# Kernel tuning notes

Hardware: AMD Instinct MI355X
Metric: run time of the kernel (lower is better)

## Reference

```python
import jax, jax.numpy as jnp
import numpy as np

B = 16384       # batch size
P = 2           # fixed pooling factor per bag (offsets are arange * P)
NTAB = 26       # number of sparse feature tables
NROWS = 100000  # rows per embedding table
D = 128         # embedding dim == ln_bot[-1]
LN_BOT = [13, 512, 256, 128]
LN_TOP = [479, 1024, 512, 256, 1]


def setup_inputs() -> dict:
    key = jax.random.key(0)
    ks = jax.random.split(key, 32)
    inp = {}
    inp['dense_x'] = jax.random.normal(ks[0], (B, LN_BOT[0]), dtype=jnp.float32)
    # offsets: uniform stride-P bags (EmbeddingBag offsets)
    inp['lS_o'] = jnp.broadcast_to(jnp.arange(B, dtype=jnp.int64) * P, (NTAB, B))
    inp['lS_i'] = jax.random.randint(ks[1], (NTAB, B * P), 0, NROWS, dtype=jnp.int64)
    # embedding tables, uniform(-sqrt(1/n), sqrt(1/n))
    bound = float(np.sqrt(1.0 / NROWS))
    inp['emb_tables'] = jax.random.uniform(ks[2], (NTAB, NROWS, D), dtype=jnp.float32,
                                           minval=-bound, maxval=bound)
    # bot MLP params (He-style scaled normal)
    ki = 3
    for i in range(len(LN_BOT) - 1):
        n, m = LN_BOT[i], LN_BOT[i + 1]
        inp[f'bw{i}'] = jax.random.normal(ks[ki], (m, n), dtype=jnp.float32) * np.sqrt(2.0 / (m + n)); ki += 1
        inp[f'bb{i}'] = jax.random.normal(ks[ki], (m,), dtype=jnp.float32) * np.sqrt(1.0 / m); ki += 1
    for i in range(len(LN_TOP) - 1):
        n, m = LN_TOP[i], LN_TOP[i + 1]
        inp[f'tw{i}'] = jax.random.normal(ks[ki], (m, n), dtype=jnp.float32) * np.sqrt(2.0 / (m + n)); ki += 1
        inp[f'tb{i}'] = jax.random.normal(ks[ki], (m,), dtype=jnp.float32) * np.sqrt(1.0 / m); ki += 1
    return inp


def _mlp(x, Ws, bs, sigmoid_layer):
    for i, (W, b) in enumerate(zip(Ws, bs)):
        x = x @ W.T + b
        x = jax.nn.sigmoid(x) if i == sigmoid_layer else jax.nn.relu(x)
    return x


def reference(dense_x, lS_o, lS_i, emb_tables,
              bw0, bb0, bw1, bb1, bw2, bb2,
              tw0, tb0, tw1, tb1, tw2, tb2, tw3, tb3):
    # bot MLP (sigmoid_bot = -1 -> all ReLU)
    x = _mlp(dense_x, [bw0, bw1, bw2], [bb0, bb1, bb2], sigmoid_layer=-1)  # [B, D]

    # multi-table EmbeddingBag sum pooling. Offsets (lS_o) are uniform stride-P
    # arange bags, so sum pooling is a gather + reshape + sum over P.
    def pool_one(table, idx):
        return table[idx].reshape(B, P, D).sum(axis=1)  # [B, D]
    ly = jax.vmap(pool_one)(emb_tables, lS_i)  # [NTAB, B, D]

    # dot interaction (arch_interaction_itself=False -> strict lower triangle)
    T = jnp.concatenate([x[:, None, :], jnp.transpose(ly, (1, 0, 2))], axis=1)  # [B, 27, D]
    Z = jnp.einsum('bid,bjd->bij', T, T)  # [B, 27, 27]
    ni = NTAB + 1
    li, lj = jnp.tril_indices(ni, k=-1)
    Zflat = Z[:, li, lj]  # [B, 351]
    R = jnp.concatenate([x, Zflat], axis=1)  # [B, 479]

    # top MLP (sigmoid at last layer, sigmoid_top = 3)
    p = _mlp(R, [tw0, tw1, tw2, tw3], [tb0, tb1, tb2, tb3], sigmoid_layer=3)
    return p  # [B, 1]
```

## Files before the change

### kernel.cpp

```cpp
#include <hip/hip_runtime.h>
#include <hip/hip_bf16.h>
#include <math.h>

#define BATCH 16384
#define NTAB 26
#define DIM 128
#define NROWS 100000

typedef short bf16x8 __attribute__((ext_vector_type(8)));
typedef float f32x4 __attribute__((ext_vector_type(4)));
typedef float f32x16 __attribute__((ext_vector_type(16)));

__device__ __forceinline__ ushort f2b(float f) {
  union { float f; unsigned u; } c; c.f = f;
  unsigned r = (c.u + 0x7fffu + ((c.u >> 16) & 1u)) >> 16;
  return (ushort)r;
}
__device__ __forceinline__ float b2f(ushort u) {
  union { unsigned u; float f; } c; c.u = (unsigned)u << 16;
  return c.f;
}

__device__ __forceinline__ void gload_lds16(const void* g, void* l) {
  __builtin_amdgcn_global_load_lds(
      (const __attribute__((address_space(1))) void*)g,
      (__attribute__((address_space(3))) void*)l, 16, 0, 0);
}

__global__ __launch_bounds__(256) void prep_kernel(
    const float* __restrict__ x, const float* __restrict__ W0,
    const float* __restrict__ b0, ushort* __restrict__ y,
    const float* __restrict__ bw1, const float* __restrict__ bw2,
    const float* __restrict__ tw0, const float* __restrict__ tw1,
    const float* __restrict__ tw2,
    ushort* __restrict__ o1, ushort* __restrict__ o2, ushort* __restrict__ o3,
    ushort* __restrict__ o4, ushort* __restrict__ o5) {
  int blk = blockIdx.x;
  if (blk < 2 * BATCH) {
    int b = blk >> 1;
    int m = ((blk & 1) << 8) | threadIdx.x;
    const float* xr = x + (size_t)b * 13;
    const float* wr = W0 + (size_t)m * 13;
    float acc = b0[m];
#pragma unroll
    for (int k = 0; k < 13; k++) acc = fmaf(xr[k], wr[k], acc);
    y[(size_t)b * 512 + m] = f2b(fmaxf(acc, 0.f));
    return;
  }
  int cb = blk - 2 * BATCH;
  int c = cb >> 11;
  int i = (cb & 2047) * 256 + threadIdx.x;
  switch (c) {
    case 0: if (i < 256 * 512) o1[i] = f2b(bw1[i]); break;
    case 1: if (i < 128 * 256) {
      int r = i >> 8, cc = i & 255;
      int db = (((cc << 1) ^ ((r & 7) << 4)) >> 1);
      o2[r * 256 + db] = f2b(bw2[i]);
    } break;
    case 2: if (i < 1024 * 512) {
      int r = i >> 9, cc = i & 511;
      o3[i] = (cc < 479) ? f2b(tw0[(size_t)r * 479 + cc]) : (ushort)0;
    } break;
    case 3: if (i < 512 * 1024) o4[i] = f2b(tw1[i]); break;
    case 4: if (i < 256 * 512) o5[i] = f2b(tw2[i]); break;
  }
}

__global__ __launch_bounds__(256) void embint_kernel(
    const float* __restrict__ tables, const int* __restrict__ lS_i,
    const ushort* __restrict__ xb, ushort* __restrict__ R) {
  __shared__ ushort Tls[4][32 * 128];
  const int wave = threadIdx.x >> 6, lane = threadIdx.x & 63;
  const int b = blockIdx.x * 4 + wave;
  char* tl = (char*)Tls[wave];

  *(uint*)(tl + lane * 4) = *(const uint*)(xb + (size_t)b * 128 + lane * 2);
#pragma unroll
  for (int r = 27; r < 32; r++)
    *(uint*)(tl + r * 256 + ((lane * 4) ^ ((r & 7) << 4))) = 0;
#pragma unroll 8
  for (int t = 0; t < NTAB; t++) {
    const int* idx = lS_i + ((size_t)t << 15) + (b << 1);
    int i0 = idx[0], i1 = idx[1];
    float2 v0 = ((const float2*)(tables + ((size_t)t * NROWS + i0) * DIM))[lane];
    float2 v1 = ((const float2*)(tables + ((size_t)t * NROWS + i1) * DIM))[lane];
    ushort2 s; s.x = f2b(v0.x + v1.x); s.y = f2b(v0.y + v1.y);
    int row = t + 1;
    *(uint*)(tl + row * 256 + ((lane * 4) ^ ((row & 7) << 4))) = *(uint*)&s;
  }
  __syncthreads();

  const int row = lane & 31;
  const int khb = (lane >> 5) * 16;
  const int swz = (row & 7) << 4;
  f32x16 z = {};
#pragma unroll
  for (int ks = 0; ks < 8; ks++) {
    bf16x8 a = *(const bf16x8*)(tl + row * 256 + ((ks * 32 + khb) ^ swz));
    z = __builtin_amdgcn_mfma_f32_32x32x16_bf16(a, a, z, 0, 0, 0);
  }

  ushort* Rb = R + (size_t)b * 512;
  *(uint*)(Rb + lane * 2) = *(const uint*)(tl + lane * 4);
  if (lane < 33) Rb[479 + lane] = 0;
  const int j = lane & 31;
  const int rb4 = (lane >> 5) * 4;
#pragma unroll
  for (int r = 0; r < 16; r++) {
    int i = (r & 3) + 8 * (r >> 2) + rb4;
    if (i <= 26 && j < i) Rb[DIM + (i * (i - 1)) / 2 + j] = f2b(z[r]);
  }
}

#define BMLP_SLOT 20480
__global__ __launch_bounds__(256) void bmlp_kernel(
    const ushort* __restrict__ A, const ushort* __restrict__ W1,
    const float* __restrict__ b1, const ushort* __restrict__ W2g,
    const float* __restrict__ b2, ushort* __restrict__ Y) {
  __shared__ char lds[3 * BMLP_SLOT + 64 * 260 * 2 + 65536];
  char* C1 = lds + 3 * BMLP_SLOT;
  char* W2s = C1 + 64 * 260 * 2;
  const int tid = threadIdx.x;
  const int lane = tid & 63, wave = tid >> 6;
  const int m0 = blockIdx.x * 64;

  const int srow = lane >> 2;
  const int scolb = ((lane & 3) << 4) ^ ((srow & 3) << 4);

#pragma unroll
  for (int i = 0; i < 16; i++)
    gload_lds16(W2g + i * 2048 + wave * 512 + lane * 8, W2s + i * 4096 + wave * 1024);

#pragma unroll
  for (int kt = 0; kt < 2; kt++) {
    char* As = lds + kt * BMLP_SLOT;
    char* W1s = As + 4096;
    const int k0 = kt * 32;
    gload_lds16(A + (size_t)(m0 + wave * 16 + srow) * 512 + k0 + (scolb >> 1),
                As + wave * 1024);
#pragma unroll
    for (int i = 0; i < 4; i++)
      gload_lds16(W1 + (size_t)(wave * 64 + i * 16 + srow) * 512 + k0 + (scolb >> 1),
                  W1s + wave * 4096 + i * 1024);
  }

  f32x4 acc1[4][4] = {};
  const int fr = lane & 15;
  const int fkb = (lane >> 4) * 16;
  const int fswz = (fr & 3) << 4;

  for (int kt = 0; kt < 16; kt++) {
    if (kt < 15) { asm volatile("s_waitcnt vmcnt(5)" ::: "memory"); }
    else         { asm volatile("s_waitcnt vmcnt(0)" ::: "memory"); }
    __builtin_amdgcn_sched_barrier(0);
    __builtin_amdgcn_s_barrier();
    __builtin_amdgcn_sched_barrier(0);

    const char* As = lds + (kt % 3) * BMLP_SLOT;
    const char* W1s = As + 4096;
    bf16x8 a[4], w[4];
#pragma unroll
    for (int i = 0; i < 4; i++)
      a[i] = *(const bf16x8*)(As + (i * 16 + fr) * 64 + (fkb ^ fswz));
#pragma unroll
    for (int j = 0; j < 4; j++)
      w[j] = *(const bf16x8*)(W1s + (wave * 64 + j * 16 + fr) * 64 + (fkb ^ fswz));

    if (kt + 2 < 16) {
      char* Ad = lds + ((kt + 2) % 3) * BMLP_SLOT;
      char* W1d = Ad + 4096;
      const int k2 = (kt + 2) * 32;
      gload_lds16(A + (size_t)(m0 + wave * 16 + srow) * 512 + k2 + (scolb >> 1),
                  Ad + wave * 1024);
#pragma unroll
      for (int i = 0; i < 4; i++)
        gload_lds16(W1 + (size_t)(wave * 64 + i * 16 + srow) * 512 + k2 + (scolb >> 1),
                    W1d + wave * 4096 + i * 1024);
    }

    asm volatile("s_waitcnt lgkmcnt(0)" ::: "memory");
    __builtin_amdgcn_sched_barrier(0);
    __builtin_amdgcn_s_setprio(1);
#pragma unroll
    for (int i = 0; i < 4; i++)
#pragma unroll
      for (int j = 0; j < 4; j++)
        acc1[i][j] = __builtin_amdgcn_mfma_f32_16x16x32_bf16(a[i], w[j], acc1[i][j], 0, 0, 0);
    __builtin_amdgcn_s_setprio(0);
  }

  const int col_l = lane & 15, row_h = (lane >> 4) * 4;
#pragma unroll
  for (int j = 0; j < 4; j++) {
    int n = wave * 64 + j * 16 + col_l;
    float bs = b1[n];
#pragma unroll
    for (int i = 0; i < 4; i++) {
      int rw = i * 16 + row_h;
#pragma unroll
      for (int r = 0; r < 4; r++)
        *(ushort*)(C1 + (size_t)(rw + r) * 520 + n * 2) = f2b(fmaxf(acc1[i][j][r] + bs, 0.f));
    }
  }
  __syncthreads();

  f32x4 acc2[4][2] = {};
#pragma unroll
  for (int ks = 0; ks < 8; ks++) {
    const int kb = ks * 64 + fkb;
    bf16x8 a2[4], w2[2];
#pragma unroll
    for (int i = 0; i < 4; i++)
      a2[i] = *(const bf16x8*)(C1 + (i * 16 + fr) * 520 + kb);
#pragma unroll
    for (int j = 0; j < 2; j++)
      w2[j] = *(const bf16x8*)(W2s + (wave * 32 + j * 16 + fr) * 512 + (kb ^ ((fr & 7) << 4)));
#pragma unroll
    for (int i = 0; i < 4; i++)
#pragma unroll
      for (int j = 0; j < 2; j++)
        acc2[i][j] = __builtin_amdgcn_mfma_f32_16x16x32_bf16(a2[i], w2[j], acc2[i][j], 0, 0, 0);
  }

#pragma unroll
  for (int j = 0; j < 2; j++) {
    int n = wave * 32 + j * 16 + col_l;
    float bs = b2[n];
#pragma unroll
    for (int i = 0; i < 4; i++) {
      int mb = m0 + i * 16 + row_h;
#pragma unroll
      for (int r = 0; r < 4; r++)
        Y[(size_t)(mb + r) * 128 + n] = f2b(fmaxf(acc2[i][j][r] + bs, 0.f));
    }
  }
}

#define SLOT_BYTES 49152
template <int ACT>
__global__ __launch_bounds__(512, 2) void gemm256_kernel(
    const ushort* __restrict__ A, const ushort* __restrict__ W,
    const float* __restrict__ bias, ushort* __restrict__ C, int K, int ldc) {
  __shared__ char lds[3 * SLOT_BYTES];
  const int tid = threadIdx.x;
  const int lane = tid & 63, wid = tid >> 6;
  const int wm = wid >> 2, wn = wid & 3;

  const int nwg = gridDim.x * gridDim.y;
  const int orig = blockIdx.y * gridDim.x + blockIdx.x;
  const int q = nwg >> 3, r8 = nwg & 7;
  const int xcd = orig & 7, pos = orig >> 3;
  const int swzid = (xcd < r8 ? xcd * (q + 1) : r8 * (q + 1) + (xcd - r8) * q) + pos;
  const int m0 = (swzid / gridDim.x) * 256, n0 = (swzid % gridDim.x) * 128;
  const int NK = K >> 6;

  const int srow = tid >> 3;
  const int scolb = (tid & 7) << 4;

#pragma unroll
  for (int kt = 0; kt < 2; kt++) {
    char* As = lds + kt * SLOT_BYTES;
    char* Bs = As + 32768;
    const int k0 = kt * 64;
#pragma unroll
    for (int i = 0; i < 4; i++) {
      int row = i * 64 + srow;
      int colb = scolb ^ ((row & 7) << 4);
      gload_lds16(A + (size_t)(m0 + row) * K + k0 + (colb >> 1), As + i * 8192 + wid * 1024);
    }
#pragma unroll
    for (int i = 0; i < 2; i++) {
      int row = i * 64 + srow;
      int colb = scolb ^ ((row & 7) << 4);
      gload_lds16(W + (size_t)(n0 + row) * K + k0 + (colb >> 1), Bs + i * 8192 + wid * 1024);
    }
  }

  f32x4 acc[8][2] = {};
  const int fr = lane & 15;
  const int fkb = (lane >> 4) * 16;

  for (int kt = 0; kt < NK; kt++) {
    if (kt + 1 < NK) { asm volatile("s_waitcnt vmcnt(6)" ::: "memory"); }
    else             { asm volatile("s_waitcnt vmcnt(0)" ::: "memory"); }
    __builtin_amdgcn_sched_barrier(0);
    __builtin_amdgcn_s_barrier();
    __builtin_amdgcn_sched_barrier(0);

    const char* As = lds + (kt % 3) * SLOT_BYTES;
    const char* Bs = As + 32768;
    char* Ad = lds + ((kt + 2) % 3) * SLOT_BYTES;
    char* Bd = Ad + 32768;
    const int k2 = (kt + 2) * 64;
    const bool do_stage = (kt + 2 < NK);

#pragma unroll
    for (int kh = 0; kh < 2; kh++) {
      bf16x8 a[8], b[2];
#pragma unroll
      for (int mf = 0; mf < 8; mf++) {
        int row = wm * 128 + mf * 16 + fr;
        int colb = (kh * 64 + fkb) ^ ((row & 7) << 4);
        a[mf] = *(const bf16x8*)(As + row * 128 + colb);
      }
#pragma unroll
      for (int nf = 0; nf < 2; nf++) {
        int row = wn * 32 + nf * 16 + fr;
        int colb = (kh * 64 + fkb) ^ ((row & 7) << 4);
        b[nf] = *(const bf16x8*)(Bs + row * 128 + colb);
      }
      if (do_stage) {
#pragma unroll
        for (int i = kh * 2; i < kh * 2 + 2; i++) {
          int row = i * 64 + srow;
          int colb = scolb ^ ((row & 7) << 4);
          gload_lds16(A + (size_t)(m0 + row) * K + k2 + (colb >> 1), Ad + i * 8192 + wid * 1024);
        }
        {
          int row = kh * 64 + srow;
          int colb = scolb ^ ((row & 7) << 4);
          gload_lds16(W + (size_t)(n0 + row) * K + k2 + (colb >> 1), Bd + kh * 8192 + wid * 1024);
        }
      }
      __builtin_amdgcn_sched_barrier(0);
      __builtin_amdgcn_s_barrier();
      asm volatile("s_waitcnt lgkmcnt(0)" ::: "memory");
      __builtin_amdgcn_sched_barrier(0);
      __builtin_amdgcn_s_setprio(1);
#pragma unroll
      for (int mf = 0; mf < 8; mf++)
#pragma unroll
        for (int nf = 0; nf < 2; nf++)
          acc[mf][nf] = __builtin_amdgcn_mfma_f32_16x16x32_bf16(a[mf], b[nf], acc[mf][nf], 0, 0, 0);
      __builtin_amdgcn_s_setprio(0);
      if (kh == 0) {
        __builtin_amdgcn_sched_barrier(0);
        __builtin_amdgcn_s_barrier();
        __builtin_amdgcn_sched_barrier(0);
      }
    }
  }

  const int cr = lane & 15, rh = (lane >> 4) * 4;
#pragma unroll
  for (int nf = 0; nf < 2; nf++) {
    int n = n0 + wn * 32 + nf * 16 + cr;
    float bs = bias[n];
#pragma unroll
    for (int mf = 0; mf < 8; mf++) {
      int mb = m0 + wm * 128 + mf * 16 + rh;
#pragma unroll
      for (int r = 0; r < 4; r++) {
        float v = acc[mf][nf][r] + bs;
        if (ACT) v = fmaxf(v, 0.f);
        C[(size_t)(mb + r) * ldc + n] = f2b(v);
      }
    }
  }
}

__global__ __launch_bounds__(256) void t2final_kernel(
    const ushort* __restrict__ A, const ushort* __restrict__ W,
    const float* __restrict__ bias, const float* __restrict__ w3,
    const float* __restrict__ b3, float* __restrict__ out) {
  __shared__ char smem[64 * 264 * 2];
  ushort* As = (ushort*)smem;
  ushort* Bs = (ushort*)(smem + 4096);
  ushort* Ct = (ushort*)smem;
  const int tid = threadIdx.x;
  const int lane = tid & 63, wave = tid >> 6;
  const int m0 = blockIdx.x * 64;

  const int srow = lane >> 2;
  const int scolb = ((lane & 3) << 4) ^ ((srow & 3) << 4);
  const ushort* Ag = A + (size_t)(m0 + wave * 16 + srow) * 512 + (scolb >> 1);
  const ushort* Wg = W + (size_t)(wave * 16 + srow) * 512 + (scolb >> 1);

  f32x4 acc[4][4] = {};
  const int fr = lane & 15;
  const int fkb = (lane >> 4) * 16;
  const int fswz = (fr & 3) << 4;

  for (int k0 = 0; k0 < 512; k0 += 32) {
    gload_lds16(Ag + k0, (char*)As + wave * 1024);
#pragma unroll
    for (int i = 0; i < 4; i++)
      gload_lds16(Wg + (size_t)(i * 64) * 512 + k0, (char*)Bs + i * 4096 + wave * 1024);
    __syncthreads();
    bf16x8 a[4], b[4];
#pragma unroll
    for (int i = 0; i < 4; i++) {
      a[i] = *(const bf16x8*)((const char*)As + (i * 16 + fr) * 64 + (fkb ^ fswz));
      b[i] = *(const bf16x8*)((const char*)Bs + (wave * 64 + i * 16 + fr) * 64 + (fkb ^ fswz));
    }
#pragma unroll
    for (int i = 0; i < 4; i++)
#pragma unroll
      for (int j = 0; j < 4; j++)
        acc[i][j] = __builtin_amdgcn_mfma_f32_16x16x32_bf16(a[i], b[j], acc[i][j], 0, 0, 0);
    __syncthreads();
  }

  const int col_l = lane & 15, row_h = (lane >> 4) * 4;
#pragma unroll
  for (int j = 0; j < 4; j++) {
    int n = wave * 64 + j * 16 + col_l;
    float bs = bias[n];
#pragma unroll
    for (int i = 0; i < 4; i++) {
      int mb = i * 16 + row_h;
#pragma unroll
      for (int r = 0; r < 4; r++)
        Ct[(size_t)(mb + r) * 264 + n] = f2b(fmaxf(acc[i][j][r] + bs, 0.f));
    }
  }
  __syncthreads();

  const float4 wv = ((const float4*)w3)[lane];
  const float bf = b3[0];
  for (int rr = 0; rr < 16; rr++) {
    int row = wave * 16 + rr;
    ushort4 a4 = *(const ushort4*)&Ct[(size_t)row * 264 + lane * 4];
    float s = b2f(a4.x) * wv.x + b2f(a4.y) * wv.y + b2f(a4.z) * wv.z + b2f(a4.w) * wv.w;
#pragma unroll
    for (int off = 32; off >= 1; off >>= 1) s += __shfl_xor(s, off);
    if (lane == 0) out[m0 + row] = 1.f / (1.f + expf(-(s + bf)));
  }
}

extern "C" void kernel_launch(void* const* d_in, const int* in_sizes, int n_in,
                              void* d_out, int out_size, void* d_ws, size_t ws_size,
                              hipStream_t stream) {
  const float* dense_x = (const float*)d_in[0];
  const int* lS_i = (const int*)d_in[2];
  const float* emb = (const float*)d_in[3];
  const float* bw0 = (const float*)d_in[4];
  const float* bb0 = (const float*)d_in[5];
  const float* bw1 = (const float*)d_in[6];
  const float* bb1 = (const float*)d_in[7];
  const float* bw2 = (const float*)d_in[8];
  const float* bb2 = (const float*)d_in[9];
  const float* tw0 = (const float*)d_in[10];
  const float* tb0 = (const float*)d_in[11];
  const float* tw1 = (const float*)d_in[12];
  const float* tb1 = (const float*)d_in[13];
  const float* tw2 = (const float*)d_in[14];
  const float* tb2 = (const float*)d_in[15];
  const float* tw3 = (const float*)d_in[16];
  const float* tb3 = (const float*)d_in[17];
  float* out = (float*)d_out;

  char* w = (char*)d_ws;
  ushort* xb  = (ushort*)w; w += (size_t)BATCH * 128 * 2;
  ushort* x1  = (ushort*)w; w += (size_t)BATCH * 512 * 2;
  ushort* x2  = (ushort*)w; w += (size_t)BATCH * 256 * 2;
  ushort* R   = (ushort*)w; w += (size_t)BATCH * 512 * 2;
  ushort* t1  = (ushort*)w; w += (size_t)BATCH * 1024 * 2;
  ushort* wb1 = (ushort*)w; w += 256 * 512 * 2;
  ushort* wb2 = (ushort*)w; w += 128 * 256 * 2;
  ushort* wt0 = (ushort*)w; w += 1024 * 512 * 2;
  ushort* wt1 = (ushort*)w; w += 512 * 1024 * 2;
  ushort* wt2 = (ushort*)w; w += 256 * 512 * 2;
  ushort* t2 = x1;
  (void)x2;

  prep_kernel<<<2 * BATCH + 5 * 2048, 256, 0, stream>>>(
      dense_x, bw0, bb0, x1, bw1, bw2, tw0, tw1, tw2, wb1, wb2, wt0, wt1, wt2);

  bmlp_kernel<<<BATCH / 64, 256, 0, stream>>>(x1, wb1, bb1, wb2, bb2, xb);

  embint_kernel<<<BATCH / 4, 256, 0, stream>>>(emb, lS_i, xb, R);

  gemm256_kernel<1><<<dim3(1024 / 128, BATCH / 256), 512, 0, stream>>>(R,  wt0, tb0, t1, 512, 1024);
  gemm256_kernel<1><<<dim3(512 / 128,  BATCH / 256), 512, 0, stream>>>(t1, wt1, tb1, t2, 1024, 512);
  t2final_kernel<<<BATCH / 64, 256, 0, stream>>>(t2, wt2, tb2, tw3, tb3, out);
}
```

Before: 204.8 us.

## Fuse first bottom-MLP layer into bmlp kernel via padded bf16 MFMA

Moves the 13→512 bottom-MLP layer out of the scalar prep kernel and into the bottom-MLP kernel. The dense input and first-layer weights are padded to K=32 in bf16 and multiplied with MFMA, with the 512-wide activation kept in swizzled LDS instead of being written to and re-read from global memory. LDS is reorganised so the W2 buffer reuses the layer-1 activation region once it is dead, and biases are preloaded into registers. This removes a 16 MB global round trip and a large scalar-FMA launch. In exchange the dense input is quantised to bf16 before the first layer and the LDS reuse needs careful barriers.

```diff
diff --git a/kernel.cpp b/kernel.cpp
--- a/kernel.cpp
+++ b/kernel.cpp
@@ -28,29 +28,15 @@
 }
 
 __global__ __launch_bounds__(256) void prep_kernel(
-    const float* __restrict__ x, const float* __restrict__ W0,
-    const float* __restrict__ b0, ushort* __restrict__ y,
+    const float* __restrict__ dense_x, const float* __restrict__ bw0,
     const float* __restrict__ bw1, const float* __restrict__ bw2,
     const float* __restrict__ tw0, const float* __restrict__ tw1,
     const float* __restrict__ tw2,
+    ushort* __restrict__ dxp, ushort* __restrict__ wb0,
     ushort* __restrict__ o1, ushort* __restrict__ o2, ushort* __restrict__ o3,
     ushort* __restrict__ o4, ushort* __restrict__ o5) {
-  int blk = blockIdx.x;
-  if (blk < 2 * BATCH) {
-    int b = blk >> 1;
-    int m = ((blk & 1) << 8) | threadIdx.x;
-    const float* xr = x + (size_t)b * 13;
-    const float* wr = W0 + (size_t)m * 13;
-    float acc = b0[m];
-#pragma unroll
-    for (int k = 0; k < 13; k++) acc = fmaf(xr[k], wr[k], acc);
-    y[(size_t)b * 512 + m] = f2b(fmaxf(acc, 0.f));
-    return;
-  }
-  int cb = blk - 2 * BATCH;
-  int c = cb >> 11;
-  int i = (cb & 2047) * 256 + threadIdx.x;
-  switch (c) {
+  int i = blockIdx.x * 256 + threadIdx.x;
+  switch (blockIdx.y) {
     case 0: if (i < 256 * 512) o1[i] = f2b(bw1[i]); break;
     case 1: if (i < 128 * 256) {
       int r = i >> 8, cc = i & 255;
@@ -63,6 +49,14 @@
     } break;
     case 3: if (i < 512 * 1024) o4[i] = f2b(tw1[i]); break;
     case 4: if (i < 256 * 512) o5[i] = f2b(tw2[i]); break;
+    case 5: if (i < BATCH * 32) {
+      int r = i >> 5, c = i & 31;
+      dxp[i] = (c < 13) ? f2b(dense_x[r * 13 + c]) : (ushort)0;
+    } break;
+    case 6: if (i < 512 * 32) {
+      int r = i >> 5, c = i & 31;
+      wb0[i] = (c < 13) ? f2b(bw0[r * 13 + c]) : (ushort)0;
+    } break;
   }
 }
 
@@ -112,70 +106,121 @@
   }
 }
 
-#define BMLP_SLOT 20480
+#define RING_SLOT 16384
 __global__ __launch_bounds__(256) void bmlp_kernel(
-    const ushort* __restrict__ A, const ushort* __restrict__ W1,
+    const ushort* __restrict__ dxp, const ushort* __restrict__ wb0,
+    const float* __restrict__ b0, const ushort* __restrict__ W1,
     const float* __restrict__ b1, const ushort* __restrict__ W2g,
     const float* __restrict__ b2, ushort* __restrict__ Y) {
-  __shared__ char lds[3 * BMLP_SLOT + 64 * 260 * 2 + 65536];
-  char* C1 = lds + 3 * BMLP_SLOT;
-  char* W2s = C1 + 64 * 260 * 2;
+  __shared__ char lds[65536 + 3 * RING_SLOT + 36864];
+  char* R1 = lds;
+  char* RING = lds + 65536;
+  char* wb0s = lds + 65536 + 3 * RING_SLOT;
+  char* dxt = wb0s + 32768;
   const int tid = threadIdx.x;
   const int lane = tid & 63, wave = tid >> 6;
   const int m0 = blockIdx.x * 64;
+  const int fr = lane & 15;
+  const int kqb = (lane >> 4) * 16;
+  const int cl = lane & 15, rh = (lane >> 4) * 4;
+
+  float vb0[8], vb1[4], vb2[2];
+#pragma unroll
+  for (int h = 0; h < 2; h++)
+#pragma unroll
+    for (int nf = 0; nf < 4; nf++)
+      vb0[h * 4 + nf] = b0[wave * 128 + h * 64 + nf * 16 + cl];
+#pragma unroll
+  for (int j = 0; j < 4; j++) vb1[j] = b1[wave * 64 + j * 16 + cl];
+#pragma unroll
+  for (int j = 0; j < 2; j++) vb2[j] = b2[wave * 32 + j * 16 + cl];
+
+#pragma unroll
+  for (int i = 0; i < 8; i++) {
+    int flat = i * 4096 + tid * 16;
+    int row = flat >> 6, cb = flat & 63;
+    gload_lds16(wb0 + row * 32 + (cb >> 1), wb0s + flat);
+  }
+  {
+    int flat = tid * 16;
+    int row = flat >> 6, cb = flat & 63;
+    gload_lds16(dxp + (size_t)(m0 + row) * 32 + (cb >> 1), dxt + flat);
+  }
 
   const int srow = lane >> 2;
   const int scolb = ((lane & 3) << 4) ^ ((srow & 3) << 4);
-
-#pragma unroll
-  for (int i = 0; i < 16; i++)
-    gload_lds16(W2g + i * 2048 + wave * 512 + lane * 8, W2s + i * 4096 + wave * 1024);
-
-#pragma unroll
-  for (int kt = 0; kt < 2; kt++) {
-    char* As = lds + kt * BMLP_SLOT;
-    char* W1s = As + 4096;
-    const int k0 = kt * 32;
-    gload_lds16(A + (size_t)(m0 + wave * 16 + srow) * 512 + k0 + (scolb >> 1),
-                As + wave * 1024);
+#pragma unroll
+  for (int kt = 0; kt < 2; kt++)
 #pragma unroll
     for (int i = 0; i < 4; i++)
-      gload_lds16(W1 + (size_t)(wave * 64 + i * 16 + srow) * 512 + k0 + (scolb >> 1),
-                  W1s + wave * 4096 + i * 1024);
-  }
+      gload_lds16(W1 + (size_t)(wave * 64 + i * 16 + srow) * 512 + kt * 32 + (scolb >> 1),
+                  RING + kt * RING_SLOT + wave * 4096 + i * 1024);
+
+  asm volatile("s_waitcnt vmcnt(8)" ::: "memory");
+  __builtin_amdgcn_sched_barrier(0);
+  __builtin_amdgcn_s_barrier();
+  __builtin_amdgcn_sched_barrier(0);
+
+  {
+    bf16x8 a0[4];
+#pragma unroll
+    for (int mf = 0; mf < 4; mf++)
+      a0[mf] = *(const bf16x8*)(dxt + (mf * 16 + fr) * 64 + kqb);
+#pragma unroll
+    for (int h = 0; h < 2; h++) {
+      f32x4 acc0[4][4] = {};
+#pragma unroll
+      for (int nf = 0; nf < 4; nf++) {
+        int wrow = wave * 128 + h * 64 + nf * 16 + fr;
+        bf16x8 bb = *(const bf16x8*)(wb0s + wrow * 64 + kqb);
+#pragma unroll
+        for (int mf = 0; mf < 4; mf++)
+          acc0[mf][nf] = __builtin_amdgcn_mfma_f32_16x16x32_bf16(a0[mf], bb, acc0[mf][nf], 0, 0, 0);
+      }
+#pragma unroll
+      for (int nf = 0; nf < 4; nf++) {
+        int n = wave * 128 + h * 64 + nf * 16 + cl;
+#pragma unroll
+        for (int mf = 0; mf < 4; mf++)
+#pragma unroll
+          for (int r = 0; r < 4; r++) {
+            int row = mf * 16 + rh + r;
+            float v = fmaxf(acc0[mf][nf][r] + vb0[h * 4 + nf], 0.f);
+            *(ushort*)(R1 + row * 1024 + ((2 * n) ^ ((row & 7) << 4))) = f2b(v);
+          }
+      }
+    }
+  }
+  asm volatile("s_waitcnt lgkmcnt(0)" ::: "memory");
+  __builtin_amdgcn_sched_barrier(0);
+  __builtin_amdgcn_s_barrier();
+  __builtin_amdgcn_sched_barrier(0);
 
   f32x4 acc1[4][4] = {};
-  const int fr = lane & 15;
-  const int fkb = (lane >> 4) * 16;
   const int fswz = (fr & 3) << 4;
-
   for (int kt = 0; kt < 16; kt++) {
-    if (kt < 15) { asm volatile("s_waitcnt vmcnt(5)" ::: "memory"); }
+    if (kt < 15) { asm volatile("s_waitcnt vmcnt(4)" ::: "memory"); }
     else         { asm volatile("s_waitcnt vmcnt(0)" ::: "memory"); }
     __builtin_amdgcn_sched_barrier(0);
     __builtin_amdgcn_s_barrier();
     __builtin_amdgcn_sched_barrier(0);
 
-    const char* As = lds + (kt % 3) * BMLP_SLOT;
-    const char* W1s = As + 4096;
+    const char* W1s = RING + (kt % 3) * RING_SLOT;
     bf16x8 a[4], w[4];
 #pragma unroll
-    for (int i = 0; i < 4; i++)
-      a[i] = *(const bf16x8*)(As + (i * 16 + fr) * 64 + (fkb ^ fswz));
+    for (int i = 0; i < 4; i++) {
+      int row = i * 16 + fr;
+      a[i] = *(const bf16x8*)(R1 + row * 1024 + ((kt * 64 + kqb) ^ ((row & 7) << 4)));
+    }
 #pragma unroll
     for (int j = 0; j < 4; j++)
-      w[j] = *(const bf16x8*)(W1s + (wave * 64 + j * 16 + fr) * 64 + (fkb ^ fswz));
+      w[j] = *(const bf16x8*)(W1s + (wave * 64 + j * 16 + fr) * 64 + (kqb ^ fswz));
 
     if (kt + 2 < 16) {
-      char* Ad = lds + ((kt + 2) % 3) * BMLP_SLOT;
-      char* W1d = Ad + 4096;
-      const int k2 = (kt + 2) * 32;
-      gload_lds16(A + (size_t)(m0 + wave * 16 + srow) * 512 + k2 + (scolb >> 1),
-                  Ad + wave * 1024);
 #pragma unroll
       for (int i = 0; i < 4; i++)
-        gload_lds16(W1 + (size_t)(wave * 64 + i * 16 + srow) * 512 + k2 + (scolb >> 1),
-                    W1d + wave * 4096 + i * 1024);
+        gload_lds16(W1 + (size_t)(wave * 64 + i * 16 + srow) * 512 + (kt + 2) * 32 + (scolb >> 1),
+                    RING + ((kt + 2) % 3) * RING_SLOT + wave * 4096 + i * 1024);
     }
 
     asm volatile("s_waitcnt lgkmcnt(0)" ::: "memory");
@@ -189,17 +234,22 @@
     __builtin_amdgcn_s_setprio(0);
   }
 
-  const int col_l = lane & 15, row_h = (lane >> 4) * 4;
+  __builtin_amdgcn_s_barrier();
+
+#pragma unroll
+  for (int i = 0; i < 16; i++)
+    gload_lds16(W2g + i * 2048 + tid * 8, R1 + i * 4096 + tid * 16);
+
+  char* C1 = RING;
 #pragma unroll
   for (int j = 0; j < 4; j++) {
-    int n = wave * 64 + j * 16 + col_l;
-    float bs = b1[n];
+    int n = wave * 64 + j * 16 + cl;
 #pragma unroll
     for (int i = 0; i < 4; i++) {
-      int rw = i * 16 + row_h;
+      int rw = i * 16 + rh;
 #pragma unroll
       for (int r = 0; r < 4; r++)
-        *(ushort*)(C1 + (size_t)(rw + r) * 520 + n * 2) = f2b(fmaxf(acc1[i][j][r] + bs, 0.f));
+        *(ushort*)(C1 + (size_t)(rw + r) * 520 + n * 2) = f2b(fmaxf(acc1[i][j][r] + vb1[j], 0.f));
     }
   }
   __syncthreads();
@@ -207,31 +257,29 @@
   f32x4 acc2[4][2] = {};
 #pragma unroll
   for (int ks = 0; ks < 8; ks++) {
-    const int kb = ks * 64 + fkb;
+    const int kb = ks * 64 + kqb;
     bf16x8 a2[4], w2[2];
 #pragma unroll
     for (int i = 0; i < 4; i++)
       a2[i] = *(const bf16x8*)(C1 + (i * 16 + fr) * 520 + kb);
 #pragma unroll
     for (int j = 0; j < 2; j++)
-      w2[j] = *(const bf16x8*)(W2s + (wave * 32 + j * 16 + fr) * 512 + (kb ^ ((fr & 7) << 4)));
+      w2[j] = *(const bf16x8*)(R1 + (wave * 32 + j * 16 + fr) * 512 + (kb ^ ((fr & 7) << 4)));
 #pragma unroll
     for (int i = 0; i < 4; i++)
 #pragma unroll
       for (int j = 0; j < 2; j++)
         acc2[i][j] = __builtin_amdgcn_mfma_f32_16x16x32_bf16(a2[i], w2[j], acc2[i][j], 0, 0, 0);
   }
-
 #pragma unroll
   for (int j = 0; j < 2; j++) {
-    int n = wave * 32 + j * 16 + col_l;
-    float bs = b2[n];
+    int n = wave * 32 + j * 16 + cl;
 #pragma unroll
     for (int i = 0; i < 4; i++) {
-      int mb = m0 + i * 16 + row_h;
+      int mb = m0 + i * 16 + rh;
 #pragma unroll
       for (int r = 0; r < 4; r++)
-        Y[(size_t)(mb + r) * 128 + n] = f2b(fmaxf(acc2[i][j][r] + bs, 0.f));
+        Y[(size_t)(mb + r) * 128 + n] = f2b(fmaxf(acc2[i][j][r] + vb2[j], 0.f));
     }
   }
 }
@@ -461,13 +509,16 @@
   ushort* wt0 = (ushort*)w; w += 1024 * 512 * 2;
   ushort* wt1 = (ushort*)w; w += 512 * 1024 * 2;
   ushort* wt2 = (ushort*)w; w += 256 * 512 * 2;
+  ushort* dxp = (ushort*)w; w += (size_t)BATCH * 32 * 2;
+  ushort* wb0 = (ushort*)w; w += 512 * 32 * 2;
   ushort* t2 = x1;
   (void)x2;
 
-  prep_kernel<<<2 * BATCH + 5 * 2048, 256, 0, stream>>>(
-      dense_x, bw0, bb0, x1, bw1, bw2, tw0, tw1, tw2, wb1, wb2, wt0, wt1, wt2);
-
-  bmlp_kernel<<<BATCH / 64, 256, 0, stream>>>(x1, wb1, bb1, wb2, bb2, xb);
+  prep_kernel<<<dim3(2048, 7), 256, 0, stream>>>(
+      dense_x, bw0, bw1, bw2, tw0, tw1, tw2, dxp, wb0,
+      wb1, wb2, wt0, wt1, wt2);
+
+  bmlp_kernel<<<BATCH / 64, 256, 0, stream>>>(dxp, wb0, bb0, wb1, bb1, wb2, bb2, xb);
 
   embint_kernel<<<BATCH / 4, 256, 0, stream>>>(emb, lS_i, xb, R);
 
```

Result: faster. 186.6 us (-8.9%).
